# Kernel tuning notes

Measured on AMD Instinct MI355X. Metric: run time of the kernel, lower is better.

The kernel has to match this reference:

```python
import jax, jax.numpy as jnp
import numpy as np

N_NODES = 100000
N_EDGES = 1600000
D_IN = 128
D_OUT = 128


def setup_inputs() -> dict:
    key = jax.random.key(0)
    k1, k2, k3, k4, k5 = jax.random.split(key, 5)
    h = jax.random.normal(k1, (N_NODES, D_IN), dtype=jnp.float32)
    src = jax.random.randint(k2, (N_EDGES,), 0, N_NODES, dtype=jnp.int64)
    dst = jax.random.randint(k3, (N_EDGES,), 0, N_NODES, dtype=jnp.int64)
    W = jax.random.normal(k4, (2 * D_IN, D_OUT), dtype=jnp.float32) * (1.0 / np.sqrt(2 * D_IN))
    b = jax.random.normal(k5, (D_OUT,), dtype=jnp.float32) * 0.01
    return {"h": h, "src": src, "dst": dst, "W": W, "b": b}


def reference(h, src, dst, W, b):
    # copy_u + mean: scatter-mean of source features onto destination nodes
    msg_sum = jax.ops.segment_sum(h[src], dst, num_segments=N_NODES)  # [N, D_IN]
    deg = jax.ops.segment_sum(jnp.ones((src.shape[0],), h.dtype), dst, num_segments=N_NODES)  # [N]
    h_N = jnp.where(deg[:, None] > 0, msg_sum / jnp.maximum(deg, 1.0)[:, None], 0.0)
    h_total = jnp.concatenate([h, h_N], axis=1)  # [N, 2*D_IN]
    return h_total @ W + b
```

## Files before the change

### kernel.cpp

```cpp
#include <hip/hip_runtime.h>
#include <stdint.h>

#define N_NODES 100000
#define D 128
#define BN 64
#define NB ((N_NODES + BN - 1) / BN)
#define EPB 4096
#define NR 4
#define CAPR 448
#define CAP 1536
#define HPAD 136
#define NK 512

typedef short bf16x8 __attribute__((ext_vector_type(8)));
typedef float f32x4 __attribute__((ext_vector_type(4)));

__device__ __forceinline__ unsigned short f2bf(float f) {
    unsigned int x = __float_as_uint(f);
    unsigned int r = x + 0x7fffu + ((x >> 16) & 1u);
    return (unsigned short)(r >> 16);
}
__device__ __forceinline__ float blo(unsigned int u) { return __uint_as_float(u << 16); }
__device__ __forceinline__ float bhi(unsigned int u) { return __uint_as_float(u & 0xffff0000u); }

__global__ __launch_bounds__(256) void prep_k(
    const float* __restrict__ h, unsigned short* __restrict__ h_bf,
    const float* __restrict__ W, unsigned short* __restrict__ Wf,
    const int* __restrict__ src, const int* __restrict__ dst,
    int* __restrict__ cnt, unsigned int* __restrict__ pairs,
    int n_edges, int partb)
{
    __shared__ int hist[NB];
    __shared__ int lc[NB];

    int bid = blockIdx.x;
    int t = threadIdx.x;

    if (bid < partb) {
        for (int i = t; i < NB; i += 256) { hist[i] = 0; lc[i] = 0; }
        __syncthreads();
        int base = bid * EPB;
        int lim = n_edges - base; if (lim > EPB) lim = EPB; if (lim < 0) lim = 0;
        for (int i = t; i < lim; i += 256)
            atomicAdd(&hist[dst[base + i] >> 6], 1);
        __syncthreads();
        int rep = bid & (NR - 1);
        for (int i = t; i < NB; i += 256) {
            int c = hist[i];
            hist[i] = c ? atomicAdd(&cnt[i * NR + rep], c) : 0;
        }
        __syncthreads();
        for (int i = t; i < lim; i += 256) {
            int e = base + i;
            int d = dst[e], b = d >> 6;
            int slot = atomicAdd(&lc[b], 1);
            int off = hist[b] + slot;
            if (off < CAPR)
                pairs[((size_t)b * NR + rep) * CAPR + off] =
                    (unsigned int)src[e] | ((unsigned int)(d & 63) << 17);
        }
    } else if (bid < partb + 16) {
        int gid = (bid - partb) * 256 + t;
        if (gid < 64 * 64) {
            int f = gid >> 6, l = gid & 63;
            int kt = f >> 3, ct = f & 7;
            int n = ct * 16 + (l & 15);
            int kb = kt * 32 + (l >> 4) * 8;
            #pragma unroll
            for (int j = 0; j < 8; ++j)
                Wf[(size_t)f * 512 + l * 8 + j] = f2bf(W[(size_t)(kb + j) * D + n]);
        }
    } else {
        size_t base = ((size_t)(bid - partb - 16) * 256 + t) * 4;
        if (base < (size_t)N_NODES * D) {
            float4 v = *(const float4*)(h + base);
            ushort4 o;
            o.x = f2bf(v.x); o.y = f2bf(v.y); o.z = f2bf(v.z); o.w = f2bf(v.w);
            *(ushort4*)(h_bf + base) = o;
        }
    }
}

__global__ __launch_bounds__(512, 8) void aggemm_k(
    const unsigned short* __restrict__ h_bf, const unsigned int* __restrict__ pairs,
    const int* __restrict__ cnt_g, const unsigned short* __restrict__ Wf,
    const float* __restrict__ bias, float* __restrict__ out)
{
    __shared__ unsigned int lp[CAP];
    __shared__ unsigned int srt[CAP];
    __shared__ int cnt2[NK];
    __shared__ int ps[NK];
    __shared__ int cur2[NK];
    __shared__ int counts[BN];
    __shared__ int startp[BN];
    __shared__ unsigned short hNs[BN][HPAD];

    int t = threadIdx.x;
    int b = blockIdx.x;
    int wv = t >> 6, l = t & 63;

    int segc[NR], sego[NR];
    {
        int tot = 0;
        #pragma unroll
        for (int r = 0; r < NR; ++r) {
            int c = cnt_g[b * NR + r];
            if (c > CAPR) c = CAPR;
            if (tot + c > CAP) c = CAP - tot;
            sego[r] = tot; segc[r] = c; tot += c;
        }
    }

    cnt2[t] = 0;
    __syncthreads();

    #pragma unroll
    for (int r = 0; r < NR; ++r) {
        const unsigned int* psg = pairs + ((size_t)b * NR + r) * CAPR;
        int c = segc[r], o = sego[r];
        for (int i = t; i < c; i += 512) {
            unsigned int p = psg[i];
            lp[o + i] = p;
            atomicAdd(&cnt2[p >> 14], 1);
        }
    }
    int cnt = sego[NR - 1] + segc[NR - 1];
    __syncthreads();

    ps[t] = cnt2[t];
    __syncthreads();
    #pragma unroll
    for (int off = 1; off < NK; off <<= 1) {
        int v = (t >= off) ? ps[t - off] : 0;
        __syncthreads();
        ps[t] += v;
        __syncthreads();
    }
    int excl = ps[t] - cnt2[t];
    cur2[t] = excl;
    if ((t & 7) == 0) startp[t >> 3] = excl;
    __syncthreads();
    if ((t & 7) == 7) counts[t >> 3] = ps[t] - startp[t >> 3];
    __syncthreads();

    for (int i = t; i < cnt; i += 512) {
        unsigned int p = lp[i];
        int s = atomicAdd(&cur2[p >> 14], 1);
        srt[s] = p & 0x1FFFFu;
    }
    __syncthreads();

    int q = l >> 4, lq = l & 15;
    int nbase = b * BN;
    #pragma unroll
    for (int p2 = 0; p2 < 2; ++p2) {
        int nl = p2 * 32 + wv * 4 + q;
        int dg = counts[nl], s0 = startp[nl];
        float a0 = 0.f, a1 = 0.f, a2 = 0.f, a3 = 0.f;
        float a4 = 0.f, a5 = 0.f, a6 = 0.f, a7 = 0.f;
        int i = 0;
        for (; i + 4 <= dg; i += 4) {
            int s0i = srt[s0 + i],     s1i = srt[s0 + i + 1];
            int s2i = srt[s0 + i + 2], s3i = srt[s0 + i + 3];
            uint4 u0 = *(const uint4*)(h_bf + (size_t)s0i * D + lq * 8);
            uint4 u1 = *(const uint4*)(h_bf + (size_t)s1i * D + lq * 8);
            uint4 u2 = *(const uint4*)(h_bf + (size_t)s2i * D + lq * 8);
            uint4 u3 = *(const uint4*)(h_bf + (size_t)s3i * D + lq * 8);
            a0 += (blo(u0.x) + blo(u1.x)) + (blo(u2.x) + blo(u3.x));
            a1 += (bhi(u0.x) + bhi(u1.x)) + (bhi(u2.x) + bhi(u3.x));
            a2 += (blo(u0.y) + blo(u1.y)) + (blo(u2.y) + blo(u3.y));
            a3 += (bhi(u0.y) + bhi(u1.y)) + (bhi(u2.y) + bhi(u3.y));
            a4 += (blo(u0.z) + blo(u1.z)) + (blo(u2.z) + blo(u3.z));
            a5 += (bhi(u0.z) + bhi(u1.z)) + (bhi(u2.z) + bhi(u3.z));
            a6 += (blo(u0.w) + blo(u1.w)) + (blo(u2.w) + blo(u3.w));
            a7 += (bhi(u0.w) + bhi(u1.w)) + (bhi(u2.w) + bhi(u3.w));
        }
        for (; i < dg; ++i) {
            uint4 u = *(const uint4*)(h_bf + (size_t)srt[s0 + i] * D + lq * 8);
            a0 += blo(u.x); a1 += bhi(u.x);
            a2 += blo(u.y); a3 += bhi(u.y);
            a4 += blo(u.z); a5 += bhi(u.z);
            a6 += blo(u.w); a7 += bhi(u.w);
        }
        float invd = dg > 0 ? 1.0f / (float)dg : 0.f;
        uint4 o;
        o.x = ((unsigned int)f2bf(a1 * invd) << 16) | f2bf(a0 * invd);
        o.y = ((unsigned int)f2bf(a3 * invd) << 16) | f2bf(a2 * invd);
        o.z = ((unsigned int)f2bf(a5 * invd) << 16) | f2bf(a4 * invd);
        o.w = ((unsigned int)f2bf(a7 * invd) << 16) | f2bf(a6 * invd);
        *(uint4*)(&hNs[nl][lq * 8]) = o;
    }
    __syncthreads();

    int rt = wv >> 1, ch = wv & 1;
    int lrow = l & 15, lqd = l >> 4;
    int lr = rt * 16 + lrow;
    int r0 = nbase + lr; if (r0 > N_NODES - 1) r0 = N_NODES - 1;

    f32x4 acc[4];
    #pragma unroll
    for (int c = 0; c < 4; ++c) acc[c] = (f32x4){0.f, 0.f, 0.f, 0.f};

    const unsigned short* wf_lane = Wf + l * 8;

    #pragma unroll
    for (int kt = 0; kt < 8; ++kt) {
        int ko = (kt & 3) * 32 + lqd * 8;
        bf16x8 a;
        if (kt < 4)
            a = *(const bf16x8*)(h_bf + (size_t)r0 * D + ko);
        else
            a = *(const bf16x8*)(&hNs[lr][ko]);
        #pragma unroll
        for (int c = 0; c < 4; ++c) {
            int ct = ch * 4 + c;
            bf16x8 bfr = *(const bf16x8*)(wf_lane + (size_t)(kt * 8 + ct) * 512);
            acc[c] = __builtin_amdgcn_mfma_f32_16x16x32_bf16(a, bfr, acc[c], 0, 0, 0);
        }
    }

    int col = l & 15, qd = l >> 4;
    #pragma unroll
    for (int c = 0; c < 4; ++c) {
        int ct = ch * 4 + c;
        float bv = bias[ct * 16 + col];
        #pragma unroll
        for (int r = 0; r < 4; ++r) {
            int row = nbase + rt * 16 + qd * 4 + r;
            if (row < N_NODES)
                out[(size_t)row * D + ct * 16 + col] = acc[c][r] + bv;
        }
    }
}


extern "C" void kernel_launch(void* const* d_in, const int* in_sizes, int n_in,
                              void* d_out, int out_size, void* d_ws, size_t ws_size,
                              hipStream_t stream) {
    const float* h  = (const float*)d_in[0];
    const int* src  = (const int*)d_in[1];
    const int* dst  = (const int*)d_in[2];
    const float* W  = (const float*)d_in[3];
    const float* b  = (const float*)d_in[4];
    float* out      = (float*)d_out;
    int n_edges = in_sizes[1];

    char* ws = (char*)d_ws;
    unsigned short* h_bf  = (unsigned short*)ws;
    unsigned int* pairs   = (unsigned int*)(h_bf + (size_t)N_NODES * D);
    unsigned short* Wf    = (unsigned short*)(pairs + (size_t)NB * NR * CAPR);
    int* cnt              = (int*)(Wf + 64 * 512);

    hipMemsetAsync(cnt, 0, NB * NR * sizeof(int), stream);

    int partb = (n_edges + EPB - 1) / EPB;
    int cblocks = (int)(((size_t)N_NODES * D / 4 + 255) / 256);
    hipLaunchKernelGGL(prep_k, dim3(partb + 16 + cblocks), dim3(256), 0, stream,
                       h, h_bf, W, Wf, src, dst, cnt, pairs, n_edges, partb);

    hipLaunchKernelGGL(aggemm_k, dim3(NB), dim3(512), 0, stream,
                       h_bf, pairs, cnt, Wf, b, out);
}
```

Before: 222.1 us.

## Fuse prep and aggregation-GEMM into one persistent cooperative kernel with work queues

Merges the memset, the preprocessing kernel and the aggregate+GEMM kernel into a single persistent cooperative kernel. Two atomic work queues distribute items and a grid-wide sync separates the phases. The aggregation sort now bins per destination node, with 64 bins instead of 512 and a shorter scan. Each node's segment is padded to a multiple of 4 and filled with a zero row, so the gather loop reads indices as vectors, unrolls by 8 and needs no scalar tail. This removes launch and memset overhead and shrinks the in-block sort, at the cost of grid.sync, per-item atomics and possibly lower occupancy from the larger shared-memory union.

```diff
diff --git a/kernel.cpp b/kernel.cpp
--- a/kernel.cpp
+++ b/kernel.cpp
@@ -1,5 +1,8 @@
 #include <hip/hip_runtime.h>
+#include <hip/hip_cooperative_groups.h>
 #include <stdint.h>
+
+namespace cg = cooperative_groups;
 
 #define N_NODES 100000
 #define D 128
@@ -9,8 +12,10 @@
 #define NR 4
 #define CAPR 448
 #define CAP 1536
+#define CAPS 1792
 #define HPAD 136
-#define NK 512
+#define ZROW N_NODES
+#define NCONV 6250
 
 typedef short bf16x8 __attribute__((ext_vector_type(8)));
 typedef float f32x4 __attribute__((ext_vector_type(4)));
@@ -23,212 +28,232 @@
 __device__ __forceinline__ float blo(unsigned int u) { return __uint_as_float(u << 16); }
 __device__ __forceinline__ float bhi(unsigned int u) { return __uint_as_float(u & 0xffff0000u); }
 
-__global__ __launch_bounds__(256) void prep_k(
+__global__ __launch_bounds__(512, 6) void fused_k(
     const float* __restrict__ h, unsigned short* __restrict__ h_bf,
     const float* __restrict__ W, unsigned short* __restrict__ Wf,
     const int* __restrict__ src, const int* __restrict__ dst,
     int* __restrict__ cnt, unsigned int* __restrict__ pairs,
-    int n_edges, int partb)
+    const float* __restrict__ bias, float* __restrict__ out,
+    int* __restrict__ wq, int n_edges, int partb)
 {
-    __shared__ int hist[NB];
-    __shared__ int lc[NB];
-
-    int bid = blockIdx.x;
+    __shared__ union {
+        struct { int hist[NB]; int lc[NB]; } a;
+        struct {
+            unsigned int lp[CAP];
+            unsigned int srt[CAPS];
+            int cnt2[BN], sb[BN], startp[BN], cur2[BN];
+            unsigned short hNs[BN][HPAD];
+        } b;
+    } sm;
+    __shared__ int curw;
+
+    cg::grid_group grid = cg::this_grid();
     int t = threadIdx.x;
-
-    if (bid < partb) {
-        for (int i = t; i < NB; i += 256) { hist[i] = 0; lc[i] = 0; }
-        __syncthreads();
-        int base = bid * EPB;
-        int lim = n_edges - base; if (lim > EPB) lim = EPB; if (lim < 0) lim = 0;
-        for (int i = t; i < lim; i += 256)
-            atomicAdd(&hist[dst[base + i] >> 6], 1);
-        __syncthreads();
-        int rep = bid & (NR - 1);
-        for (int i = t; i < NB; i += 256) {
-            int c = hist[i];
-            hist[i] = c ? atomicAdd(&cnt[i * NR + rep], c) : 0;
-        }
-        __syncthreads();
-        for (int i = t; i < lim; i += 256) {
-            int e = base + i;
-            int d = dst[e], b = d >> 6;
-            int slot = atomicAdd(&lc[b], 1);
-            int off = hist[b] + slot;
-            if (off < CAPR)
-                pairs[((size_t)b * NR + rep) * CAPR + off] =
-                    (unsigned int)src[e] | ((unsigned int)(d & 63) << 17);
-        }
-    } else if (bid < partb + 16) {
-        int gid = (bid - partb) * 256 + t;
-        if (gid < 64 * 64) {
-            int f = gid >> 6, l = gid & 63;
-            int kt = f >> 3, ct = f & 7;
-            int n = ct * 16 + (l & 15);
-            int kb = kt * 32 + (l >> 4) * 8;
-            #pragma unroll
-            for (int j = 0; j < 8; ++j)
-                Wf[(size_t)f * 512 + l * 8 + j] = f2bf(W[(size_t)(kb + j) * D + n]);
-        }
-    } else {
-        size_t base = ((size_t)(bid - partb - 16) * 256 + t) * 4;
-        if (base < (size_t)N_NODES * D) {
+    size_t gtid = (size_t)blockIdx.x * 512 + t;
+    size_t gsz = (size_t)gridDim.x * 512;
+
+    for (size_t i = gtid; i < (size_t)NB * NR; i += gsz) cnt[i] = 0;
+    if (gtid < 64) ((unsigned int*)(h_bf + (size_t)ZROW * D))[gtid] = 0;
+    if (gtid < 2) wq[gtid] = 0;
+    grid.sync();
+
+    int nitems = partb + NCONV + 1;
+    for (;;) {
+        if (t == 0) curw = atomicAdd(&wq[0], 1);
+        __syncthreads();
+        int it = curw;
+        __syncthreads();
+        if (it >= nitems) break;
+
+        if (it < partb) {
+            for (int i = t; i < NB; i += 512) { sm.a.hist[i] = 0; sm.a.lc[i] = 0; }
+            __syncthreads();
+            int base = it * EPB;
+            int lim = n_edges - base; if (lim > EPB) lim = EPB; if (lim < 0) lim = 0;
+            for (int i = t; i < lim; i += 512)
+                atomicAdd(&sm.a.hist[dst[base + i] >> 6], 1);
+            __syncthreads();
+            int rep = it & (NR - 1);
+            for (int i = t; i < NB; i += 512) {
+                int c = sm.a.hist[i];
+                sm.a.hist[i] = c ? atomicAdd(&cnt[i * NR + rep], c) : 0;
+            }
+            __syncthreads();
+            for (int i = t; i < lim; i += 512) {
+                int e = base + i;
+                int d = dst[e], bk = d >> 6;
+                int slot = atomicAdd(&sm.a.lc[bk], 1);
+                int off = sm.a.hist[bk] + slot;
+                if (off < CAPR)
+                    pairs[((size_t)bk * NR + rep) * CAPR + off] =
+                        (unsigned int)src[e] | ((unsigned int)(d & 63) << 17);
+            }
+            __syncthreads();
+        } else if (it < partb + NCONV) {
+            size_t base = ((size_t)(it - partb) * 512 + t) * 4;
             float4 v = *(const float4*)(h + base);
             ushort4 o;
             o.x = f2bf(v.x); o.y = f2bf(v.y); o.z = f2bf(v.z); o.w = f2bf(v.w);
             *(ushort4*)(h_bf + base) = o;
+        } else {
+            for (int g = t; g < 4096; g += 512) {
+                int f = g >> 6, l = g & 63;
+                int kt = f >> 3, ct = f & 7;
+                int n = ct * 16 + (l & 15);
+                int kb = kt * 32 + (l >> 4) * 8;
+                #pragma unroll
+                for (int j = 0; j < 8; ++j)
+                    Wf[(size_t)f * 512 + l * 8 + j] = f2bf(W[(size_t)(kb + j) * D + n]);
+            }
         }
     }
-}
-
-__global__ __launch_bounds__(512, 8) void aggemm_k(
-    const unsigned short* __restrict__ h_bf, const unsigned int* __restrict__ pairs,
-    const int* __restrict__ cnt_g, const unsigned short* __restrict__ Wf,
-    const float* __restrict__ bias, float* __restrict__ out)
-{
-    __shared__ unsigned int lp[CAP];
-    __shared__ unsigned int srt[CAP];
-    __shared__ int cnt2[NK];
-    __shared__ int ps[NK];
-    __shared__ int cur2[NK];
-    __shared__ int counts[BN];
-    __shared__ int startp[BN];
-    __shared__ unsigned short hNs[BN][HPAD];
-
-    int t = threadIdx.x;
-    int b = blockIdx.x;
+    __threadfence();
+    grid.sync();
+
     int wv = t >> 6, l = t & 63;
-
-    int segc[NR], sego[NR];
-    {
+    int q = l >> 4, lq = l & 15;
+
+    for (;;) {
+        if (t == 0) curw = atomicAdd(&wq[1], 1);
+        __syncthreads();
+        int b = curw;
+        __syncthreads();
+        if (b >= NB) break;
+
+        int segc[NR], sego[NR];
         int tot = 0;
         #pragma unroll
         for (int r = 0; r < NR; ++r) {
-            int c = cnt_g[b * NR + r];
+            int c = cnt[b * NR + r];
             if (c > CAPR) c = CAPR;
             if (tot + c > CAP) c = CAP - tot;
             sego[r] = tot; segc[r] = c; tot += c;
         }
-    }
-
-    cnt2[t] = 0;
-    __syncthreads();
-
-    #pragma unroll
-    for (int r = 0; r < NR; ++r) {
-        const unsigned int* psg = pairs + ((size_t)b * NR + r) * CAPR;
-        int c = segc[r], o = sego[r];
-        for (int i = t; i < c; i += 512) {
-            unsigned int p = psg[i];
-            lp[o + i] = p;
-            atomicAdd(&cnt2[p >> 14], 1);
-        }
-    }
-    int cnt = sego[NR - 1] + segc[NR - 1];
-    __syncthreads();
-
-    ps[t] = cnt2[t];
-    __syncthreads();
-    #pragma unroll
-    for (int off = 1; off < NK; off <<= 1) {
-        int v = (t >= off) ? ps[t - off] : 0;
-        __syncthreads();
-        ps[t] += v;
-        __syncthreads();
-    }
-    int excl = ps[t] - cnt2[t];
-    cur2[t] = excl;
-    if ((t & 7) == 0) startp[t >> 3] = excl;
-    __syncthreads();
-    if ((t & 7) == 7) counts[t >> 3] = ps[t] - startp[t >> 3];
-    __syncthreads();
-
-    for (int i = t; i < cnt; i += 512) {
-        unsigned int p = lp[i];
-        int s = atomicAdd(&cur2[p >> 14], 1);
-        srt[s] = p & 0x1FFFFu;
-    }
-    __syncthreads();
-
-    int q = l >> 4, lq = l & 15;
-    int nbase = b * BN;
-    #pragma unroll
-    for (int p2 = 0; p2 < 2; ++p2) {
-        int nl = p2 * 32 + wv * 4 + q;
-        int dg = counts[nl], s0 = startp[nl];
-        float a0 = 0.f, a1 = 0.f, a2 = 0.f, a3 = 0.f;
-        float a4 = 0.f, a5 = 0.f, a6 = 0.f, a7 = 0.f;
-        int i = 0;
-        for (; i + 4 <= dg; i += 4) {
-            int s0i = srt[s0 + i],     s1i = srt[s0 + i + 1];
-            int s2i = srt[s0 + i + 2], s3i = srt[s0 + i + 3];
-            uint4 u0 = *(const uint4*)(h_bf + (size_t)s0i * D + lq * 8);
-            uint4 u1 = *(const uint4*)(h_bf + (size_t)s1i * D + lq * 8);
-            uint4 u2 = *(const uint4*)(h_bf + (size_t)s2i * D + lq * 8);
-            uint4 u3 = *(const uint4*)(h_bf + (size_t)s3i * D + lq * 8);
-            a0 += (blo(u0.x) + blo(u1.x)) + (blo(u2.x) + blo(u3.x));
-            a1 += (bhi(u0.x) + bhi(u1.x)) + (bhi(u2.x) + bhi(u3.x));
-            a2 += (blo(u0.y) + blo(u1.y)) + (blo(u2.y) + blo(u3.y));
-            a3 += (bhi(u0.y) + bhi(u1.y)) + (bhi(u2.y) + bhi(u3.y));
-            a4 += (blo(u0.z) + blo(u1.z)) + (blo(u2.z) + blo(u3.z));
-            a5 += (bhi(u0.z) + bhi(u1.z)) + (bhi(u2.z) + bhi(u3.z));
-            a6 += (blo(u0.w) + blo(u1.w)) + (blo(u2.w) + blo(u3.w));
-            a7 += (bhi(u0.w) + bhi(u1.w)) + (bhi(u2.w) + bhi(u3.w));
-        }
-        for (; i < dg; ++i) {
-            uint4 u = *(const uint4*)(h_bf + (size_t)srt[s0 + i] * D + lq * 8);
-            a0 += blo(u.x); a1 += bhi(u.x);
-            a2 += blo(u.y); a3 += bhi(u.y);
-            a4 += blo(u.z); a5 += bhi(u.z);
-            a6 += blo(u.w); a7 += bhi(u.w);
-        }
-        float invd = dg > 0 ? 1.0f / (float)dg : 0.f;
-        uint4 o;
-        o.x = ((unsigned int)f2bf(a1 * invd) << 16) | f2bf(a0 * invd);
-        o.y = ((unsigned int)f2bf(a3 * invd) << 16) | f2bf(a2 * invd);
-        o.z = ((unsigned int)f2bf(a5 * invd) << 16) | f2bf(a4 * invd);
-        o.w = ((unsigned int)f2bf(a7 * invd) << 16) | f2bf(a6 * invd);
-        *(uint4*)(&hNs[nl][lq * 8]) = o;
-    }
-    __syncthreads();
-
-    int rt = wv >> 1, ch = wv & 1;
-    int lrow = l & 15, lqd = l >> 4;
-    int lr = rt * 16 + lrow;
-    int r0 = nbase + lr; if (r0 > N_NODES - 1) r0 = N_NODES - 1;
-
-    f32x4 acc[4];
-    #pragma unroll
-    for (int c = 0; c < 4; ++c) acc[c] = (f32x4){0.f, 0.f, 0.f, 0.f};
-
-    const unsigned short* wf_lane = Wf + l * 8;
-
-    #pragma unroll
-    for (int kt = 0; kt < 8; ++kt) {
-        int ko = (kt & 3) * 32 + lqd * 8;
-        bf16x8 a;
-        if (kt < 4)
-            a = *(const bf16x8*)(h_bf + (size_t)r0 * D + ko);
-        else
-            a = *(const bf16x8*)(&hNs[lr][ko]);
+        int ec = tot;
+
+        if (t < BN) sm.b.cnt2[t] = 0;
+        for (int i = t; i < CAPS; i += 512) sm.b.srt[i] = ZROW;
+        __syncthreads();
+
+        #pragma unroll
+        for (int r = 0; r < NR; ++r) {
+            const unsigned int* psg = pairs + ((size_t)b * NR + r) * CAPR;
+            int c = segc[r], o = sego[r];
+            for (int i = t; i < c; i += 512) {
+                unsigned int p = psg[i];
+                sm.b.lp[o + i] = p;
+                atomicAdd(&sm.b.cnt2[p >> 17], 1);
+            }
+        }
+        __syncthreads();
+
+        if (t < BN) sm.b.sb[t] = (sm.b.cnt2[t] + 3) & ~3;
+        __syncthreads();
+        #pragma unroll
+        for (int off = 1; off < BN; off <<= 1) {
+            int v = 0;
+            if (t < BN && t >= off) v = sm.b.sb[t - off];
+            __syncthreads();
+            if (t < BN) sm.b.sb[t] += v;
+            __syncthreads();
+        }
+        if (t < BN) {
+            int pc = (sm.b.cnt2[t] + 3) & ~3;
+            int st = sm.b.sb[t] - pc;
+            sm.b.startp[t] = st;
+            sm.b.cur2[t] = st;
+        }
+        __syncthreads();
+
+        for (int i = t; i < ec; i += 512) {
+            unsigned int p = sm.b.lp[i];
+            int s = atomicAdd(&sm.b.cur2[p >> 17], 1);
+            sm.b.srt[s] = p & 0x1FFFFu;
+        }
+        __syncthreads();
+
+        int nbase = b * BN;
+        #pragma unroll
+        for (int p2 = 0; p2 < 2; ++p2) {
+            int nl = p2 * 32 + wv * 4 + q;
+            int dg = sm.b.cnt2[nl], s0 = sm.b.startp[nl];
+            int dgp = (dg + 3) & ~3;
+            float a0 = 0.f, a1 = 0.f, a2 = 0.f, a3 = 0.f;
+            float a4 = 0.f, a5 = 0.f, a6 = 0.f, a7 = 0.f;
+#define ACC8(u) { a0 += blo((u).x); a1 += bhi((u).x); a2 += blo((u).y); a3 += bhi((u).y); \
+                  a4 += blo((u).z); a5 += bhi((u).z); a6 += blo((u).w); a7 += bhi((u).w); }
+            int i = 0;
+            for (; i + 8 <= dgp; i += 8) {
+                uint4 ia = *(const uint4*)&sm.b.srt[s0 + i];
+                uint4 ib = *(const uint4*)&sm.b.srt[s0 + i + 4];
+                uint4 u0 = *(const uint4*)(h_bf + (size_t)ia.x * D + lq * 8);
+                uint4 u1 = *(const uint4*)(h_bf + (size_t)ia.y * D + lq * 8);
+                uint4 u2 = *(const uint4*)(h_bf + (size_t)ia.z * D + lq * 8);
+                uint4 u3 = *(const uint4*)(h_bf + (size_t)ia.w * D + lq * 8);
+                uint4 u4 = *(const uint4*)(h_bf + (size_t)ib.x * D + lq * 8);
+                uint4 u5 = *(const uint4*)(h_bf + (size_t)ib.y * D + lq * 8);
+                uint4 u6 = *(const uint4*)(h_bf + (size_t)ib.z * D + lq * 8);
+                uint4 u7 = *(const uint4*)(h_bf + (size_t)ib.w * D + lq * 8);
+                ACC8(u0); ACC8(u1); ACC8(u2); ACC8(u3);
+                ACC8(u4); ACC8(u5); ACC8(u6); ACC8(u7);
+            }
+            if (i < dgp) {
+                uint4 ia = *(const uint4*)&sm.b.srt[s0 + i];
+                uint4 u0 = *(const uint4*)(h_bf + (size_t)ia.x * D + lq * 8);
+                uint4 u1 = *(const uint4*)(h_bf + (size_t)ia.y * D + lq * 8);
+                uint4 u2 = *(const uint4*)(h_bf + (size_t)ia.z * D + lq * 8);
+                uint4 u3 = *(const uint4*)(h_bf + (size_t)ia.w * D + lq * 8);
+                ACC8(u0); ACC8(u1); ACC8(u2); ACC8(u3);
+            }
+#undef ACC8
+            float invd = dg > 0 ? 1.0f / (float)dg : 0.f;
+            uint4 o;
+            o.x = ((unsigned int)f2bf(a1 * invd) << 16) | f2bf(a0 * invd);
+            o.y = ((unsigned int)f2bf(a3 * invd) << 16) | f2bf(a2 * invd);
+            o.z = ((unsigned int)f2bf(a5 * invd) << 16) | f2bf(a4 * invd);
+            o.w = ((unsigned int)f2bf(a7 * invd) << 16) | f2bf(a6 * invd);
+            *(uint4*)(&sm.b.hNs[nl][lq * 8]) = o;
+        }
+        __syncthreads();
+
+        int rt = wv >> 1, ch = wv & 1;
+        int lrow = l & 15, lqd = l >> 4;
+        int lr = rt * 16 + lrow;
+        int r0 = nbase + lr; if (r0 > N_NODES - 1) r0 = N_NODES - 1;
+
+        f32x4 acc[4];
+        #pragma unroll
+        for (int c = 0; c < 4; ++c) acc[c] = (f32x4){0.f, 0.f, 0.f, 0.f};
+
+        const unsigned short* wf_lane = Wf + l * 8;
+
+        #pragma unroll
+        for (int kt = 0; kt < 8; ++kt) {
+            int ko = (kt & 3) * 32 + lqd * 8;
+            bf16x8 a;
+            if (kt < 4)
+                a = *(const bf16x8*)(h_bf + (size_t)r0 * D + ko);
+            else
+                a = *(const bf16x8*)(&sm.b.hNs[lr][ko]);
+            #pragma unroll
+            for (int c = 0; c < 4; ++c) {
+                int ct = ch * 4 + c;
+                bf16x8 bfr = *(const bf16x8*)(wf_lane + (size_t)(kt * 8 + ct) * 512);
+                acc[c] = __builtin_amdgcn_mfma_f32_16x16x32_bf16(a, bfr, acc[c], 0, 0, 0);
+            }
+        }
+
+        int col = l & 15, qd = l >> 4;
         #pragma unroll
         for (int c = 0; c < 4; ++c) {
             int ct = ch * 4 + c;
-            bf16x8 bfr = *(const bf16x8*)(wf_lane + (size_t)(kt * 8 + ct) * 512);
-            acc[c] = __builtin_amdgcn_mfma_f32_16x16x32_bf16(a, bfr, acc[c], 0, 0, 0);
-        }
-    }
-
-    int col = l & 15, qd = l >> 4;
-    #pragma unroll
-    for (int c = 0; c < 4; ++c) {
-        int ct = ch * 4 + c;
-        float bv = bias[ct * 16 + col];
-        #pragma unroll
-        for (int r = 0; r < 4; ++r) {
-            int row = nbase + rt * 16 + qd * 4 + r;
-            if (row < N_NODES)
-                out[(size_t)row * D + ct * 16 + col] = acc[c][r] + bv;
+            float bv = bias[ct * 16 + col];
+            #pragma unroll
+            for (int r = 0; r < 4; ++r) {
+                int row = nbase + rt * 16 + qd * 4 + r;
+                if (row < N_NODES)
+                    out[(size_t)row * D + ct * 16 + col] = acc[c][r] + bv;
+            }
         }
     }
 }
@@ -246,18 +271,29 @@
     int n_edges = in_sizes[1];
 
     char* ws = (char*)d_ws;
-    unsigned short* h_bf  = (unsigned short*)ws;
-    unsigned int* pairs   = (unsigned int*)(h_bf + (size_t)N_NODES * D);
-    unsigned short* Wf    = (unsigned short*)(pairs + (size_t)NB * NR * CAPR);
-    int* cnt              = (int*)(Wf + 64 * 512);
-
-    hipMemsetAsync(cnt, 0, NB * NR * sizeof(int), stream);
+    unsigned short* h_bf = (unsigned short*)ws;
+    unsigned int* pairs  = (unsigned int*)(h_bf + (size_t)(N_NODES + 1) * D);
+    unsigned short* Wf   = (unsigned short*)(pairs + (size_t)NB * NR * CAPR);
+    int* cnt             = (int*)(Wf + 64 * 512);
+    int* wq              = cnt + NB * NR;
 
     int partb = (n_edges + EPB - 1) / EPB;
-    int cblocks = (int)(((size_t)N_NODES * D / 4 + 255) / 256);
-    hipLaunchKernelGGL(prep_k, dim3(partb + 16 + cblocks), dim3(256), 0, stream,
-                       h, h_bf, W, Wf, src, dst, cnt, pairs, n_edges, partb);
-
-    hipLaunchKernelGGL(aggemm_k, dim3(NB), dim3(512), 0, stream,
-                       h_bf, pairs, cnt, Wf, b, out);
+
+    static int gblks = 0;
+    if (!gblks) {
+        hipDeviceProp_t prop;
+        hipGetDeviceProperties(&prop, 0);
+        int nbk = 0;
+        hipOccupancyMaxActiveBlocksPerMultiprocessor(&nbk, fused_k, 512, 0);
+        if (nbk < 1) nbk = 1;
+        gblks = nbk * prop.multiProcessorCount;
+        if (gblks > 4096) gblks = 4096;
+    }
+
+    void* args[] = {
+        (void*)&h, (void*)&h_bf, (void*)&W, (void*)&Wf, (void*)&src, (void*)&dst,
+        (void*)&cnt, (void*)&pairs, (void*)&b, (void*)&out, (void*)&wq,
+        (void*)&n_edges, (void*)&partb
+    };
+    hipLaunchCooperativeKernel((void*)fused_k, dim3(gblks), dim3(512), args, 0, stream);
 }
```

After: 478.7 us. 2.16x slower.
